# Kernel optimization log

Hardware: AMD Instinct MI355X
Metric: run time of the kernel (lower is better)

Reference implementation:

```python
import jax, jax.numpy as jnp
import numpy as np

B, T, F, H = 8, 1024, 1024, 16
DK = F // H


def setup_inputs() -> dict:
    key = jax.random.key(0)
    ks = jax.random.split(key, 12)
    s = 1.0 / np.sqrt(F)
    return {
        "query": jax.random.normal(ks[0], (B, T, F), jnp.float32),
        "key": jax.random.normal(ks[1], (B, T, F), jnp.float32),
        "value": jax.random.normal(ks[2], (B, T, F), jnp.float32),
        "mask": jnp.ones((B, T), jnp.float32),
        "Wq": jax.random.normal(ks[3], (F, F), jnp.float32) * s,
        "bq": jax.random.normal(ks[4], (F,), jnp.float32) * s,
        "Wk": jax.random.normal(ks[5], (F, F), jnp.float32) * s,
        "bk": jax.random.normal(ks[6], (F,), jnp.float32) * s,
        "Wv": jax.random.normal(ks[7], (F, F), jnp.float32) * s,
        "bv": jax.random.normal(ks[8], (F,), jnp.float32) * s,
        "Wo": jax.random.normal(ks[9], (F, F), jnp.float32) * s,
        "bo": jax.random.normal(ks[10], (F,), jnp.float32) * s,
    }


def reference(query, key, value, mask, Wq, bq, Wk, bk, Wv, bv, Wo, bo):
    # projections, split into heads: (B, H, T, DK)
    def proj(x, W, b):
        y = x @ W.T + b
        return y.reshape(B, -1, H, DK).transpose(0, 2, 1, 3)

    q = proj(query, Wq, bq)
    k = proj(key, Wk, bk)
    v = proj(value, Wv, bv)

    scores = jnp.einsum("bhqd,bhkd->bhqk", q, k) / jnp.sqrt(jnp.float32(DK))
    attn = jax.nn.softmax(scores, axis=-1)  # dropout is identity (eval / p=0)
    x = jnp.einsum("bhqk,bhkd->bhqd", attn, v)
    x = x.transpose(0, 2, 1, 3).reshape(B, -1, F)
    x = x @ Wo.T + bo
    return x * mask[..., None]
```

## Files before the change

### kernel.cpp

```cpp
#include <hip/hip_runtime.h>
#include <hip/hip_bf16.h>

typedef unsigned short u16;
typedef unsigned int u32;
typedef __attribute__((ext_vector_type(8))) short bf16x8;
typedef __attribute__((ext_vector_type(8))) unsigned short u16x8;
typedef __attribute__((ext_vector_type(4))) unsigned short u16x4;
typedef __attribute__((ext_vector_type(4))) float f32x4;

#define DEVI __device__ __forceinline__

static constexpr int Bn = 8, Tn = 1024, Fn = 1024, Hn = 16, DKn = 64;
static constexpr int Mtot = Bn * Tn;

DEVI u16 f2bf(float x) {
  unsigned u = __builtin_bit_cast(unsigned, x);
  u += 0x7fffu + ((u >> 16) & 1u);
  return (u16)(u >> 16);
}

DEVI u32 cvt_pk_bf16(float lo, float hi) {
  u32 r;
  asm("v_cvt_pk_bf16_f32 %0, %1, %2" : "=v"(r) : "v"(lo), "v"(hi));
  return r;
}

DEVI float fast_exp2(float x) { return __builtin_amdgcn_exp2f(x); }

DEVI f32x4 mfma16(bf16x8 a, bf16x8 b, f32x4 c) {
  return __builtin_amdgcn_mfma_f32_16x16x32_bf16(a, b, c, 0, 0, 0);
}

typedef const __attribute__((address_space(1))) void GAS;
typedef __attribute__((address_space(3))) void LAS;
#define GLL16(gp, lp) __builtin_amdgcn_global_load_lds((GAS*)(gp), (LAS*)(lp), 16, 0, 0)

DEVI void cvt_chunk(const float* __restrict__ in, u16* __restrict__ out, int i) {
  const float4* p = reinterpret_cast<const float4*>(in + i);
  float4 a = p[0], b = p[1];
  float v[8] = {a.x, a.y, a.z, a.w, b.x, b.y, b.z, b.w};
  u16x8 r;
#pragma unroll
  for (int j = 0; j < 8; j++) r[j] = f2bf(v[j]);
  *reinterpret_cast<u16x8*>(out + i) = r;
}

__global__ __launch_bounds__(256) void cvt3(const float* __restrict__ a, const float* __restrict__ b,
                                            const float* __restrict__ c, u16* __restrict__ oa,
                                            u16* __restrict__ ob, u16* __restrict__ oc) {
  const int id = blockIdx.x * 256 + threadIdx.x;
  const int seg = id >> 20;
  const int off = (id & 1048575) * 8;
  const float* s = seg == 0 ? a : (seg == 1 ? b : c);
  u16* d = seg == 0 ? oa : (seg == 1 ? ob : oc);
  cvt_chunk(s, d, off);
}

__global__ __launch_bounds__(256) void cvt4(const float* __restrict__ a, const float* __restrict__ b,
                                            const float* __restrict__ c, const float* __restrict__ e,
                                            u16* __restrict__ oa, u16* __restrict__ ob,
                                            u16* __restrict__ oc, u16* __restrict__ oe) {
  const int id = blockIdx.x * 256 + threadIdx.x;
  const int seg = id >> 17;
  const int off = (id & 131071) * 8;
  const float* s = seg == 0 ? a : (seg == 1 ? b : (seg == 2 ? c : e));
  u16* d = seg == 0 ? oa : (seg == 1 ? ob : (seg == 2 ? oc : oe));
  cvt_chunk(s, d, off);
}

template <int MODE>
__global__ __launch_bounds__(512, 1) void gemm8(const u16* __restrict__ A,
                                                const u16* __restrict__ Bw,
                                                const float* __restrict__ bias,
                                                const float* __restrict__ mask,
                                                u16* __restrict__ Obf,
                                                float* __restrict__ Of,
                                                float oscale) {
  constexpr int Kd = 1024;
  __shared__ u16 sA[2][256 * 64];
  __shared__ u16 sB[2][128 * 64];
  const int tid = threadIdx.x;
  const int l = tid & 63, w = tid >> 6;
  const int wm = w >> 1, wn = w & 1;
  const int lr = l & 15, g = l >> 4;
  const int bid = blockIdx.x;
  const int wg = (bid & 7) * 32 + (bid >> 3);
  const int m0 = (wg >> 3) * 256, n0 = (wg & 7) * 128;

  f32x4 acc[4][4];
#pragma unroll
  for (int i = 0; i < 4; i++)
#pragma unroll
    for (int j = 0; j < 4; j++) acc[i][j] = f32x4{0.f, 0.f, 0.f, 0.f};

  int aoff[4], boff[2];
#pragma unroll
  for (int i = 0; i < 4; i++) {
    const int c = i * 512 + tid;
    const int r = c >> 3, cc = (c & 7) ^ (r & 7);
    aoff[i] = r * Kd + cc * 8;
  }
#pragma unroll
  for (int i = 0; i < 2; i++) {
    const int c = i * 512 + tid;
    const int r = c >> 3, cc = (c & 7) ^ (r & 7);
    boff[i] = r * Kd + cc * 8;
  }
  const u16* Abase = A + (size_t)m0 * Kd;
  const u16* Bbase = Bw + (size_t)n0 * Kd;

  auto stage = [&](int buf, int kt) {
#pragma unroll
    for (int i = 0; i < 4; i++)
      GLL16(Abase + kt * 64 + aoff[i], (char*)&sA[buf][0] + (i * 512 + w * 64) * 16);
#pragma unroll
    for (int i = 0; i < 2; i++)
      GLL16(Bbase + kt * 64 + boff[i], (char*)&sB[buf][0] + (i * 512 + w * 64) * 16);
  };

  stage(0, 0);
  for (int t = 0; t < 16; ++t) {
    const int cur = t & 1;
    if (t < 15) {
      stage(cur ^ 1, t + 1);
      asm volatile("s_waitcnt vmcnt(6)" ::: "memory");
    } else {
      asm volatile("s_waitcnt vmcnt(0)" ::: "memory");
    }
    asm volatile("s_barrier" ::: "memory");
#pragma unroll
    for (int ks = 0; ks < 2; ks++) {
      bf16x8 af[4], bfr[4];
#pragma unroll
      for (int mi = 0; mi < 4; mi++) {
        const int row = wm * 64 + mi * 16 + lr;
        af[mi] = *reinterpret_cast<const bf16x8*>(
            (const char*)&sA[cur][0] + row * 128 + ((ks * 64 + g * 16) ^ ((row & 7) << 4)));
      }
#pragma unroll
      for (int ni = 0; ni < 4; ni++) {
        const int row = wn * 64 + ni * 16 + lr;
        bfr[ni] = *reinterpret_cast<const bf16x8*>(
            (const char*)&sB[cur][0] + row * 128 + ((ks * 64 + g * 16) ^ ((row & 7) << 4)));
      }
      __builtin_amdgcn_s_setprio(1);
#pragma unroll
      for (int mi = 0; mi < 4; mi++)
#pragma unroll
        for (int ni = 0; ni < 4; ni++) {
          if constexpr (MODE == 1)
            acc[mi][ni] = mfma16(af[mi], bfr[ni], acc[mi][ni]);
          else
            acc[ni][mi] = mfma16(bfr[ni], af[mi], acc[ni][mi]);
        }
      __builtin_amdgcn_s_setprio(0);
    }
    asm volatile("s_barrier" ::: "memory");
  }

  if constexpr (MODE == 1) {
#pragma unroll
    for (int ni = 0; ni < 4; ni++) {
      const int n = n0 + wn * 64 + ni * 16 + lr;
      const float bv = bias[n];
      const int h = n >> 6, dk = n & 63;
#pragma unroll
      for (int mi = 0; mi < 4; mi++) {
        const int mb = m0 + wm * 64 + mi * 16 + g * 4;
        u16x4 pk;
#pragma unroll
        for (int j = 0; j < 4; j++) pk[j] = f2bf(acc[mi][ni][j] + bv);
        const int b = mb >> 10, tt = mb & 1023;
        size_t idx = (((size_t)b * 16 + h) * 64 + dk) * 1024 + tt;
        *reinterpret_cast<u16x4*>(Obf + idx) = pk;
      }
    }
  } else {
#pragma unroll
    for (int ni = 0; ni < 4; ni++) {
      const int nb = n0 + wn * 64 + ni * 16 + g * 4;
      const float4 b4 = *reinterpret_cast<const float4*>(&bias[nb]);
#pragma unroll
      for (int mi = 0; mi < 4; mi++) {
        const int m = m0 + wm * 64 + mi * 16 + lr;
        const f32x4 a = acc[ni][mi];
        if constexpr (MODE == 0) {
          const int b = m >> 10, tt = m & 1023;
          const int h = nb >> 6, dk0 = nb & 63;
          u16x4 pk;
          pk[0] = f2bf((a[0] + b4.x) * oscale);
          pk[1] = f2bf((a[1] + b4.y) * oscale);
          pk[2] = f2bf((a[2] + b4.z) * oscale);
          pk[3] = f2bf((a[3] + b4.w) * oscale);
          *reinterpret_cast<u16x4*>(&Obf[((((size_t)b * 16 + h) * 1024 + tt) * 64) + dk0]) = pk;
        } else {
          const float mk = mask[m];
          float4 o;
          o.x = (a[0] + b4.x) * mk;
          o.y = (a[1] + b4.y) * mk;
          o.z = (a[2] + b4.z) * mk;
          o.w = (a[3] + b4.w) * mk;
          *reinterpret_cast<float4*>(&Of[(size_t)m * 1024 + nb]) = o;
        }
      }
    }
  }
}

__global__ __launch_bounds__(256, 4) void flash_attn(const u16* __restrict__ Qb,
                                                     const u16* __restrict__ Kb,
                                                     const u16* __restrict__ Vt,
                                                     u16* __restrict__ ctx) {
  __shared__ u16 sK[2][64 * 64];
  __shared__ u16 sV[64 * 64];
  __shared__ u16 pbuf[4][16 * 64];
  const int tid = threadIdx.x, l = tid & 63, w = tid >> 6;
  const int lr = l & 15, g = l >> 4;
  const int wg = ((blockIdx.x & 7) << 7) + (blockIdx.x >> 3);
  const int qt = wg & 7, bh = wg >> 3;
  const u16* Qh = Qb + (size_t)bh * (Tn * DKn);
  const u16* Kh = Kb + (size_t)bh * (Tn * DKn);
  const u16* Vh = Vt + (size_t)bh * (Tn * DKn);

  bf16x8 aq[2][2];
  int qrow[2];
#pragma unroll
  for (int qg = 0; qg < 2; qg++) {
    qrow[qg] = qt * 128 + w * 32 + qg * 16 + lr;
    aq[qg][0] = *reinterpret_cast<const bf16x8*>(Qh + (size_t)qrow[qg] * 64 + g * 8);
    aq[qg][1] = *reinterpret_cast<const bf16x8*>(Qh + (size_t)qrow[qg] * 64 + 32 + g * 8);
  }

  float mrow[2] = {-1e30f, -1e30f}, lsum[2] = {0.f, 0.f};
  f32x4 of[2][4];
#pragma unroll
  for (int qg = 0; qg < 2; qg++)
#pragma unroll
    for (int c = 0; c < 4; c++) of[qg][c] = f32x4{0.f, 0.f, 0.f, 0.f};

  char* pb = (char*)&pbuf[w][0];
  const int sw = (lr & 7) << 4;
  int wadr[4];
#pragma unroll
  for (int c = 0; c < 4; c++) wadr[c] = lr * 128 + (((c * 16 + g * 4) * 2) ^ sw);
  const int radr0 = lr * 128 + ((g * 16) ^ sw);
  const int radr1 = lr * 128 + ((64 + g * 16) ^ sw);

  auto stageK = [&](int buf, int kv0) {
#pragma unroll
    for (int i = 0; i < 2; i++) {
      const int tt = i * 256 + tid;
      const int r = tt >> 3;
      const int c = (tt & 7) ^ (r & 7);
      GLL16((const char*)Kh + ((size_t)(kv0 + r) << 7) + (c << 4),
            (char*)&sK[buf][0] + i * 4096 + w * 1024);
    }
  };
  auto stageV = [&](int kv0) {
#pragma unroll
    for (int i = 0; i < 2; i++) {
      const int tt = i * 256 + tid;
      const int r = tt >> 3;
      const int c = (tt & 7) ^ (r & 7);
      GLL16((const char*)Vh + ((size_t)r << 11) + kv0 * 2 + (c << 4),
            (char*)&sV[0] + i * 4096 + w * 1024);
    }
  };

  stageK(0, 0);
  stageV(0);
  __syncthreads();
  int cur = 0;

  for (int t = 0; t < 16; t++) {
    if (t < 15) stageK(cur ^ 1, (t + 1) * 64);
    const char* kb = (const char*)&sK[cur][0];
    const char* vb = (const char*)&sV[0];

    f32x4 sf[2][4];
    __builtin_amdgcn_s_setprio(1);
#pragma unroll
    for (int c = 0; c < 4; c++) {
      const char* kr = kb + (c * 16 + lr) * 128;
      bf16x8 k0 = *reinterpret_cast<const bf16x8*>(kr + ((g * 16) ^ sw));
      bf16x8 k1 = *reinterpret_cast<const bf16x8*>(kr + ((64 + g * 16) ^ sw));
      f32x4 z0 = mfma16(k0, aq[0][0], f32x4{0.f, 0.f, 0.f, 0.f});
      sf[0][c] = mfma16(k1, aq[0][1], z0);
      f32x4 z1 = mfma16(k0, aq[1][0], f32x4{0.f, 0.f, 0.f, 0.f});
      sf[1][c] = mfma16(k1, aq[1][1], z1);
    }
    __builtin_amdgcn_s_setprio(0);

    bf16x8 ap[2][2];
#pragma unroll
    for (int qg = 0; qg < 2; qg++) {
      f32x4 mx4 = sf[qg][0];
#pragma unroll
      for (int c = 1; c < 4; c++)
#pragma unroll
        for (int j = 0; j < 4; j++) mx4[j] = fmaxf(mx4[j], sf[qg][c][j]);
      const float pmax = fmaxf(fmaxf(mx4[0], mx4[1]), fmaxf(mx4[2], mx4[3]));
      if (__any(pmax > mrow[qg] + 8.0f)) {
        float mx = pmax;
        mx = fmaxf(mx, __shfl_xor(mx, 16));
        mx = fmaxf(mx, __shfl_xor(mx, 32));
        const float mn = fmaxf(mrow[qg], mx);
        const float alpha = fast_exp2(mrow[qg] - mn);
        mrow[qg] = mn;
        lsum[qg] *= alpha;
#pragma unroll
        for (int c = 0; c < 4; c++)
#pragma unroll
          for (int j = 0; j < 4; j++) of[qg][c][j] *= alpha;
      }
      const float mn = mrow[qg];
      float rs = 0.f;
#pragma unroll
      for (int c = 0; c < 4; c++)
#pragma unroll
        for (int j = 0; j < 4; j++) {
          float pp = fast_exp2(sf[qg][c][j] - mn);
          sf[qg][c][j] = pp;
          rs += pp;
        }
      lsum[qg] += rs;

#pragma unroll
      for (int c = 0; c < 4; c++) {
        uint2 pk;
        pk.x = cvt_pk_bf16(sf[qg][c][0], sf[qg][c][1]);
        pk.y = cvt_pk_bf16(sf[qg][c][2], sf[qg][c][3]);
        *reinterpret_cast<uint2*>(pb + wadr[c]) = pk;
      }
      ap[qg][0] = *reinterpret_cast<const bf16x8*>(pb + radr0);
      ap[qg][1] = *reinterpret_cast<const bf16x8*>(pb + radr1);
    }

    __syncthreads();

    __builtin_amdgcn_s_setprio(1);
#pragma unroll
    for (int d0 = 0; d0 < 4; d0++) {
      const char* vr = vb + (d0 * 16 + lr) * 128;
      bf16x8 v0 = *reinterpret_cast<const bf16x8*>(vr + ((g * 16) ^ sw));
      bf16x8 v1 = *reinterpret_cast<const bf16x8*>(vr + ((64 + g * 16) ^ sw));
#pragma unroll
      for (int qg = 0; qg < 2; qg++) {
        f32x4 z = mfma16(v0, ap[qg][0], of[qg][d0]);
        of[qg][d0] = mfma16(v1, ap[qg][1], z);
      }
    }
    __builtin_amdgcn_s_setprio(0);

    __syncthreads();
    if (t < 15) stageV((t + 1) * 64);
    cur ^= 1;
  }

  const int b = bh >> 4, h = bh & 15;
#pragma unroll
  for (int qg = 0; qg < 2; qg++) {
    float ls = lsum[qg];
    ls += __shfl_xor(ls, 16);
    ls += __shfl_xor(ls, 32);
    const float inv = 1.0f / ls;
    const size_t base = ((size_t)b * 1024 + qrow[qg]) * 1024 + h * 64;
#pragma unroll
    for (int d0 = 0; d0 < 4; d0++) {
      uint2 pk;
      pk.x = cvt_pk_bf16(of[qg][d0][0] * inv, of[qg][d0][1] * inv);
      pk.y = cvt_pk_bf16(of[qg][d0][2] * inv, of[qg][d0][3] * inv);
      *reinterpret_cast<uint2*>(ctx + base + d0 * 16 + g * 4) = pk;
    }
  }
}

extern "C" void kernel_launch(void* const* d_in, const int* in_sizes, int n_in,
                              void* d_out, int out_size, void* d_ws, size_t ws_size,
                              hipStream_t stream) {
  const float* query = (const float*)d_in[0];
  const float* key = (const float*)d_in[1];
  const float* value = (const float*)d_in[2];
  const float* mask = (const float*)d_in[3];
  const float* Wq = (const float*)d_in[4];
  const float* bq = (const float*)d_in[5];
  const float* Wk = (const float*)d_in[6];
  const float* bk = (const float*)d_in[7];
  const float* Wv = (const float*)d_in[8];
  const float* bv = (const float*)d_in[9];
  const float* Wo = (const float*)d_in[10];
  const float* bo = (const float*)d_in[11];
  (void)in_sizes; (void)n_in; (void)out_size; (void)ws_size;

  u16* ws = (u16*)d_ws;
  const size_t MB8 = (size_t)8 << 20;
  u16* Xq = ws;
  u16* Xk = ws + MB8;
  u16* Xv = ws + 2 * MB8;
  u16* Wqb = ws + 3 * MB8;
  u16* Wkb = Wqb + (1 << 20);
  u16* Wvb = Wkb + (1 << 20);
  u16* Wob = Wvb + (1 << 20);
  u16* Qb = Wob + (1 << 20);
  u16* Kb = Qb + MB8;
  u16* Vtb = Kb + MB8;
  u16* ctx = Xq;

  cvt3<<<12288, 256, 0, stream>>>(query, key, value, Xq, Xk, Xv);
  cvt4<<<2048, 256, 0, stream>>>(Wq, Wk, Wv, Wo, Wqb, Wkb, Wvb, Wob);

  const float SC = 0.125f * 1.44269504089f;
  const int ng = (Mtot / 256) * (Fn / 128);
  gemm8<0><<<ng, 512, 0, stream>>>(Xq, Wqb, bq, nullptr, Qb, nullptr, SC);
  gemm8<0><<<ng, 512, 0, stream>>>(Xk, Wkb, bk, nullptr, Kb, nullptr, 1.0f);
  gemm8<1><<<ng, 512, 0, stream>>>(Xv, Wvb, bv, nullptr, Vtb, nullptr, 1.0f);

  flash_attn<<<Bn * Hn * (Tn / 128), 256, 0, stream>>>(Qb, Kb, Vtb, ctx);

  gemm8<2><<<256, 512, 0, stream>>>(ctx, Wob, bo, mask, nullptr, (float*)d_out, 1.0f);
}
```

Baseline: 183.9 us.

## Fuse fp32-to-bf16 activation conversion into projection GEMM A-tile loads

Removes the separate conversion kernel for query/key/value. The projection GEMMs now load fp32 A tiles into registers, convert them with packed bf16 instructions, and write them to swizzled LDS, prefetching the next tile while the current one is computed. This avoids writing and rereading bf16 copies of the activations, at the cost of reading fp32 A through registers instead of direct global-to-LDS loads, and more register pressure. The output GEMM is split into its own non-templated kernel.

After: 176.7 us. -3.9%, faster.

```diff
diff --git a/kernel.cpp b/kernel.cpp
--- a/kernel.cpp
+++ b/kernel.cpp
@@ -43,17 +43,6 @@
 #pragma unroll
   for (int j = 0; j < 8; j++) r[j] = f2bf(v[j]);
   *reinterpret_cast<u16x8*>(out + i) = r;
-}
-
-__global__ __launch_bounds__(256) void cvt3(const float* __restrict__ a, const float* __restrict__ b,
-                                            const float* __restrict__ c, u16* __restrict__ oa,
-                                            u16* __restrict__ ob, u16* __restrict__ oc) {
-  const int id = blockIdx.x * 256 + threadIdx.x;
-  const int seg = id >> 20;
-  const int off = (id & 1048575) * 8;
-  const float* s = seg == 0 ? a : (seg == 1 ? b : c);
-  u16* d = seg == 0 ? oa : (seg == 1 ? ob : oc);
-  cvt_chunk(s, d, off);
 }
 
 __global__ __launch_bounds__(256) void cvt4(const float* __restrict__ a, const float* __restrict__ b,
@@ -69,13 +58,11 @@
 }
 
 template <int MODE>
-__global__ __launch_bounds__(512, 1) void gemm8(const u16* __restrict__ A,
-                                                const u16* __restrict__ Bw,
-                                                const float* __restrict__ bias,
-                                                const float* __restrict__ mask,
-                                                u16* __restrict__ Obf,
-                                                float* __restrict__ Of,
-                                                float oscale) {
+__global__ __launch_bounds__(512, 1) void gemm8f(const float* __restrict__ A,
+                                                 const u16* __restrict__ Bw,
+                                                 const float* __restrict__ bias,
+                                                 u16* __restrict__ Obf,
+                                                 float oscale) {
   constexpr int Kd = 1024;
   __shared__ u16 sA[2][256 * 64];
   __shared__ u16 sB[2][128 * 64];
@@ -93,6 +80,155 @@
 #pragma unroll
     for (int j = 0; j < 4; j++) acc[i][j] = f32x4{0.f, 0.f, 0.f, 0.f};
 
+  int aoffF[4], awb[4];
+#pragma unroll
+  for (int i = 0; i < 4; i++) {
+    const int c = i * 512 + tid;
+    const int r = c >> 3, cc = c & 7;
+    aoffF[i] = r * Kd + cc * 8;
+    awb[i] = r * 128 + (((cc ^ (r & 7))) << 4);
+  }
+  int boff[2];
+#pragma unroll
+  for (int i = 0; i < 2; i++) {
+    const int c = i * 512 + tid;
+    const int r = c >> 3, cc = (c & 7) ^ (r & 7);
+    boff[i] = r * Kd + cc * 8;
+  }
+  const float* Af = A + (size_t)m0 * Kd;
+  const u16* Bbase = Bw + (size_t)n0 * Kd;
+
+  float4 ra[4][2];
+  auto loadA = [&](int kt) {
+#pragma unroll
+    for (int i = 0; i < 4; i++) {
+      const float* s = Af + kt * 64 + aoffF[i];
+      ra[i][0] = *reinterpret_cast<const float4*>(s);
+      ra[i][1] = *reinterpret_cast<const float4*>(s + 4);
+    }
+  };
+  auto writeA = [&](int buf) {
+#pragma unroll
+    for (int i = 0; i < 4; i++) {
+      uint4 pk;
+      pk.x = cvt_pk_bf16(ra[i][0].x, ra[i][0].y);
+      pk.y = cvt_pk_bf16(ra[i][0].z, ra[i][0].w);
+      pk.z = cvt_pk_bf16(ra[i][1].x, ra[i][1].y);
+      pk.w = cvt_pk_bf16(ra[i][1].z, ra[i][1].w);
+      *reinterpret_cast<uint4*>((char*)&sA[buf][0] + awb[i]) = pk;
+    }
+  };
+  auto stageB = [&](int buf, int kt) {
+#pragma unroll
+    for (int i = 0; i < 2; i++)
+      GLL16(Bbase + kt * 64 + boff[i], (char*)&sB[buf][0] + (i * 512 + w * 64) * 16);
+  };
+
+  loadA(0);
+  stageB(0, 0);
+  writeA(0);
+  for (int t = 0; t < 16; ++t) {
+    const int cur = t & 1;
+    if (t < 15) {
+      loadA(t + 1);
+      stageB(cur ^ 1, t + 1);
+      asm volatile("s_waitcnt vmcnt(10) lgkmcnt(0)" ::: "memory");
+    } else {
+      asm volatile("s_waitcnt vmcnt(0) lgkmcnt(0)" ::: "memory");
+    }
+    asm volatile("s_barrier" ::: "memory");
+#pragma unroll
+    for (int ks = 0; ks < 2; ks++) {
+      bf16x8 af[4], bfr[4];
+#pragma unroll
+      for (int mi = 0; mi < 4; mi++) {
+        const int row = wm * 64 + mi * 16 + lr;
+        af[mi] = *reinterpret_cast<const bf16x8*>(
+            (const char*)&sA[cur][0] + row * 128 + ((ks * 64 + g * 16) ^ ((row & 7) << 4)));
+      }
+#pragma unroll
+      for (int ni = 0; ni < 4; ni++) {
+        const int row = wn * 64 + ni * 16 + lr;
+        bfr[ni] = *reinterpret_cast<const bf16x8*>(
+            (const char*)&sB[cur][0] + row * 128 + ((ks * 64 + g * 16) ^ ((row & 7) << 4)));
+      }
+      __builtin_amdgcn_s_setprio(1);
+#pragma unroll
+      for (int mi = 0; mi < 4; mi++)
+#pragma unroll
+        for (int ni = 0; ni < 4; ni++) {
+          if constexpr (MODE == 1)
+            acc[mi][ni] = mfma16(af[mi], bfr[ni], acc[mi][ni]);
+          else
+            acc[ni][mi] = mfma16(bfr[ni], af[mi], acc[ni][mi]);
+        }
+      __builtin_amdgcn_s_setprio(0);
+    }
+    if (t < 15) writeA(cur ^ 1);
+    asm volatile("s_barrier" ::: "memory");
+  }
+
+  if constexpr (MODE == 1) {
+#pragma unroll
+    for (int ni = 0; ni < 4; ni++) {
+      const int n = n0 + wn * 64 + ni * 16 + lr;
+      const float bv = bias[n];
+      const int h = n >> 6, dk = n & 63;
+#pragma unroll
+      for (int mi = 0; mi < 4; mi++) {
+        const int mb = m0 + wm * 64 + mi * 16 + g * 4;
+        u16x4 pk;
+#pragma unroll
+        for (int j = 0; j < 4; j++) pk[j] = f2bf(acc[mi][ni][j] + bv);
+        const int b = mb >> 10, tt = mb & 1023;
+        size_t idx = (((size_t)b * 16 + h) * 64 + dk) * 1024 + tt;
+        *reinterpret_cast<u16x4*>(Obf + idx) = pk;
+      }
+    }
+  } else {
+#pragma unroll
+    for (int ni = 0; ni < 4; ni++) {
+      const int nb = n0 + wn * 64 + ni * 16 + g * 4;
+      const float4 b4 = *reinterpret_cast<const float4*>(&bias[nb]);
+#pragma unroll
+      for (int mi = 0; mi < 4; mi++) {
+        const int m = m0 + wm * 64 + mi * 16 + lr;
+        const f32x4 a = acc[ni][mi];
+        const int b = m >> 10, tt = m & 1023;
+        const int h = nb >> 6, dk0 = nb & 63;
+        u16x4 pk;
+        pk[0] = f2bf((a[0] + b4.x) * oscale);
+        pk[1] = f2bf((a[1] + b4.y) * oscale);
+        pk[2] = f2bf((a[2] + b4.z) * oscale);
+        pk[3] = f2bf((a[3] + b4.w) * oscale);
+        *reinterpret_cast<u16x4*>(&Obf[((((size_t)b * 16 + h) * 1024 + tt) * 64) + dk0]) = pk;
+      }
+    }
+  }
+}
+
+__global__ __launch_bounds__(512, 1) void gemm_out(const u16* __restrict__ A,
+                                                   const u16* __restrict__ Bw,
+                                                   const float* __restrict__ bias,
+                                                   const float* __restrict__ mask,
+                                                   float* __restrict__ Of) {
+  constexpr int Kd = 1024;
+  __shared__ u16 sA[2][256 * 64];
+  __shared__ u16 sB[2][128 * 64];
+  const int tid = threadIdx.x;
+  const int l = tid & 63, w = tid >> 6;
+  const int wm = w >> 1, wn = w & 1;
+  const int lr = l & 15, g = l >> 4;
+  const int bid = blockIdx.x;
+  const int wg = (bid & 7) * 32 + (bid >> 3);
+  const int m0 = (wg >> 3) * 256, n0 = (wg & 7) * 128;
+
+  f32x4 acc[4][4];
+#pragma unroll
+  for (int i = 0; i < 4; i++)
+#pragma unroll
+    for (int j = 0; j < 4; j++) acc[i][j] = f32x4{0.f, 0.f, 0.f, 0.f};
+
   int aoff[4], boff[2];
 #pragma unroll
   for (int i = 0; i < 4; i++) {
@@ -147,62 +283,27 @@
 #pragma unroll
       for (int mi = 0; mi < 4; mi++)
 #pragma unroll
-        for (int ni = 0; ni < 4; ni++) {
-          if constexpr (MODE == 1)
-            acc[mi][ni] = mfma16(af[mi], bfr[ni], acc[mi][ni]);
-          else
-            acc[ni][mi] = mfma16(bfr[ni], af[mi], acc[ni][mi]);
-        }
+        for (int ni = 0; ni < 4; ni++) acc[ni][mi] = mfma16(bfr[ni], af[mi], acc[ni][mi]);
       __builtin_amdgcn_s_setprio(0);
     }
     asm volatile("s_barrier" ::: "memory");
   }
 
-  if constexpr (MODE == 1) {
-#pragma unroll
-    for (int ni = 0; ni < 4; ni++) {
-      const int n = n0 + wn * 64 + ni * 16 + lr;
-      const float bv = bias[n];
-      const int h = n >> 6, dk = n & 63;
-#pragma unroll
-      for (int mi = 0; mi < 4; mi++) {
-        const int mb = m0 + wm * 64 + mi * 16 + g * 4;
-        u16x4 pk;
-#pragma unroll
-        for (int j = 0; j < 4; j++) pk[j] = f2bf(acc[mi][ni][j] + bv);
-        const int b = mb >> 10, tt = mb & 1023;
-        size_t idx = (((size_t)b * 16 + h) * 64 + dk) * 1024 + tt;
-        *reinterpret_cast<u16x4*>(Obf + idx) = pk;
-      }
-    }
-  } else {
-#pragma unroll
-    for (int ni = 0; ni < 4; ni++) {
-      const int nb = n0 + wn * 64 + ni * 16 + g * 4;
-      const float4 b4 = *reinterpret_cast<const float4*>(&bias[nb]);
-#pragma unroll
-      for (int mi = 0; mi < 4; mi++) {
-        const int m = m0 + wm * 64 + mi * 16 + lr;
-        const f32x4 a = acc[ni][mi];
-        if constexpr (MODE == 0) {
-          const int b = m >> 10, tt = m & 1023;
-          const int h = nb >> 6, dk0 = nb & 63;
-          u16x4 pk;
-          pk[0] = f2bf((a[0] + b4.x) * oscale);
-          pk[1] = f2bf((a[1] + b4.y) * oscale);
-          pk[2] = f2bf((a[2] + b4.z) * oscale);
-          pk[3] = f2bf((a[3] + b4.w) * oscale);
-          *reinterpret_cast<u16x4*>(&Obf[((((size_t)b * 16 + h) * 1024 + tt) * 64) + dk0]) = pk;
-        } else {
-          const float mk = mask[m];
-          float4 o;
-          o.x = (a[0] + b4.x) * mk;
-          o.y = (a[1] + b4.y) * mk;
-          o.z = (a[2] + b4.z) * mk;
-          o.w = (a[3] + b4.w) * mk;
-          *reinterpret_cast<float4*>(&Of[(size_t)m * 1024 + nb]) = o;
-        }
-      }
+#pragma unroll
+  for (int ni = 0; ni < 4; ni++) {
+    const int nb = n0 + wn * 64 + ni * 16 + g * 4;
+    const float4 b4 = *reinterpret_cast<const float4*>(&bias[nb]);
+#pragma unroll
+    for (int mi = 0; mi < 4; mi++) {
+      const int m = m0 + wm * 64 + mi * 16 + lr;
+      const f32x4 a = acc[ni][mi];
+      const float mk = mask[m];
+      float4 o;
+      o.x = (a[0] + b4.x) * mk;
+      o.y = (a[1] + b4.y) * mk;
+      o.z = (a[2] + b4.z) * mk;
+      o.w = (a[3] + b4.w) * mk;
+      *reinterpret_cast<float4*>(&Of[(size_t)m * 1024 + nb]) = o;
     }
   }
 }
@@ -394,9 +495,7 @@
 
   u16* ws = (u16*)d_ws;
   const size_t MB8 = (size_t)8 << 20;
-  u16* Xq = ws;
-  u16* Xk = ws + MB8;
-  u16* Xv = ws + 2 * MB8;
+  u16* ctx = ws;
   u16* Wqb = ws + 3 * MB8;
   u16* Wkb = Wqb + (1 << 20);
   u16* Wvb = Wkb + (1 << 20);
@@ -404,18 +503,15 @@
   u16* Qb = Wob + (1 << 20);
   u16* Kb = Qb + MB8;
   u16* Vtb = Kb + MB8;
-  u16* ctx = Xq;
-
-  cvt3<<<12288, 256, 0, stream>>>(query, key, value, Xq, Xk, Xv);
+
   cvt4<<<2048, 256, 0, stream>>>(Wq, Wk, Wv, Wo, Wqb, Wkb, Wvb, Wob);
 
   const float SC = 0.125f * 1.44269504089f;
-  const int ng = (Mtot / 256) * (Fn / 128);
-  gemm8<0><<<ng, 512, 0, stream>>>(Xq, Wqb, bq, nullptr, Qb, nullptr, SC);
-  gemm8<0><<<ng, 512, 0, stream>>>(Xk, Wkb, bk, nullptr, Kb, nullptr, 1.0f);
-  gemm8<1><<<ng, 512, 0, stream>>>(Xv, Wvb, bv, nullptr, Vtb, nullptr, 1.0f);
+  gemm8f<0><<<256, 512, 0, stream>>>(query, Wqb, bq, Qb, SC);
+  gemm8f<0><<<256, 512, 0, stream>>>(key, Wkb, bk, Kb, 1.0f);
+  gemm8f<1><<<256, 512, 0, stream>>>(value, Wvb, bv, Vtb, 1.0f);
 
   flash_attn<<<Bn * Hn * (Tn / 128), 256, 0, stream>>>(Qb, Kb, Vtb, ctx);
 
-  gemm8<2><<<256, 512, 0, stream>>>(ctx, Wob, bo, mask, nullptr, (float*)d_out, 1.0f);
-}
+  gemm_out<<<256, 512, 0, stream>>>(ctx, Wob, bo, mask, (float*)d_out);
+}
```
